# Optimization experiments

Hardware: AMD Instinct MI355X
Metric: run time of the kernel (lower is better)

Reference implementation:

```python
import jax, jax.numpy as jnp
import numpy as np

N_NODES = 50000
N_PAIRS = 625000
F = 128

def setup_inputs() -> dict:
    key = jax.random.key(0)
    k1, k2, k3, k4, k5 = jax.random.split(key, 5)
    x = jax.random.normal(k1, (N_NODES, F), dtype=jnp.float32)
    alpha_ij = jax.random.normal(k2, (N_PAIRS,), dtype=jnp.float32)
    idx_i = jax.random.randint(k3, (N_PAIRS,), 0, N_NODES, dtype=jnp.int32)
    idx_j = jax.random.randint(k4, (N_PAIRS,), 0, N_NODES, dtype=jnp.int32)
    # Dense(F, use_bias=False) kernel, shape (F_in, F_out)
    W = jax.random.normal(k5, (F, F), dtype=jnp.float32) / np.sqrt(F)
    return {"x": x, "alpha_ij": alpha_ij, "idx_i": idx_i, "idx_j": idx_j, "W": W}

def reference(x, alpha_ij, idx_i, idx_j, W):
    # dense projection on nodes (n,F) @ (F,F) -> (n,F)
    v = jnp.matmul(x, W)
    # gather neighbor values, scale by attention coeff: (n_pairs, F)
    msg = alpha_ij[:, None] * v[idx_j]
    # scatter-sum back to center atoms
    return jax.ops.segment_sum(msg, segment_ids=idx_i, num_segments=x.shape[0])
```

## Files before the change

kernel.cpp:

```cpp
#include <hip/hip_runtime.h>
#include <stdint.h>

#define FDIM 128
#define BR 64
#define SLOTS 48

typedef short  s8v   __attribute__((ext_vector_type(8)));
typedef float  f4v   __attribute__((ext_vector_type(4)));
typedef unsigned short u8v __attribute__((ext_vector_type(8)));

__device__ __forceinline__ unsigned short f2bf(float f) {
    union { float f; uint32_t u; } c; c.f = f;
    uint32_t u = c.u;
    return (unsigned short)((u + 0x7fffu + ((u >> 16) & 1u)) >> 16);
}
__device__ __forceinline__ float bflo2f(uint32_t g) {
    union { uint32_t u; float f; } c; c.u = g << 16; return c.f;
}
__device__ __forceinline__ float bfhi2f(uint32_t g) {
    union { uint32_t u; float f; } c; c.u = g & 0xffff0000u; return c.f;
}

__global__ __launch_bounds__(256) void prep(const float* __restrict__ W,
                                            unsigned short* __restrict__ Wt,
                                            int* __restrict__ cnt,
                                            int n_nodes) {
    int i = blockIdx.x * 256 + threadIdx.x;
    if (i < FDIM * FDIM) {
        int n = i & 127, k = i >> 7;
        Wt[n * FDIM + k] = f2bf(W[k * FDIM + n]);
    }
    if (i < n_nodes) cnt[i] = 0;
}

__global__ __launch_bounds__(256) void gemm_mfma(const float* __restrict__ x,
                                                 const unsigned short* __restrict__ Wt,
                                                 unsigned short* __restrict__ v,
                                                 int n_rows) {
    __shared__ unsigned short As[BR][FDIM + 8];
    __shared__ unsigned short Bs[FDIM][FDIM + 8];
    const int t = threadIdx.x;
    const int row0 = blockIdx.x * BR;

    {
        int n  = t >> 1;
        int cb = (t & 1) * 64;
        const unsigned short* src = Wt + (size_t)n * FDIM + cb;
#pragma unroll
        for (int it = 0; it < 8; ++it) {
            u8v wv = *(const u8v*)(src + it * 8);
            *(u8v*)(&Bs[n][cb + it * 8]) = wv;
        }
    }
    {
        int r  = t >> 2;
        int c0 = (t & 3) * 32;
        int grow = row0 + r;
        const float* src = x + (size_t)grow * FDIM + c0;
#pragma unroll
        for (int it = 0; it < 4; ++it) {
            float4 xa = make_float4(0.f, 0.f, 0.f, 0.f);
            float4 xb = make_float4(0.f, 0.f, 0.f, 0.f);
            if (grow < n_rows) {
                xa = *(const float4*)(src + it * 8);
                xb = *(const float4*)(src + it * 8 + 4);
            }
            u8v pk;
            pk[0] = f2bf(xa.x); pk[1] = f2bf(xa.y); pk[2] = f2bf(xa.z); pk[3] = f2bf(xa.w);
            pk[4] = f2bf(xb.x); pk[5] = f2bf(xb.y); pk[6] = f2bf(xb.z); pk[7] = f2bf(xb.w);
            *(u8v*)(&As[r][c0 + it * 8]) = pk;
        }
    }
    __syncthreads();

    const int w    = t >> 6;
    const int lane = t & 63;
    const int rt   = (w & 1) * 32;
    const int ct   = (w >> 1) * 64;
    const int lrow = lane & 15;
    const int kq   = (lane >> 4) * 8;

    f4v acc[2][4];
#pragma unroll
    for (int i = 0; i < 2; ++i)
#pragma unroll
        for (int j = 0; j < 4; ++j)
            acc[i][j] = (f4v){0.f, 0.f, 0.f, 0.f};

#pragma unroll
    for (int ks = 0; ks < 4; ++ks) {
        const int k0 = ks * 32 + kq;
        s8v a0 = *(const s8v*)(&As[rt + lrow][k0]);
        s8v a1 = *(const s8v*)(&As[rt + 16 + lrow][k0]);
        s8v b0 = *(const s8v*)(&Bs[ct + lrow][k0]);
        s8v b1 = *(const s8v*)(&Bs[ct + 16 + lrow][k0]);
        s8v b2 = *(const s8v*)(&Bs[ct + 32 + lrow][k0]);
        s8v b3 = *(const s8v*)(&Bs[ct + 48 + lrow][k0]);
        acc[0][0] = __builtin_amdgcn_mfma_f32_16x16x32_bf16(a0, b0, acc[0][0], 0, 0, 0);
        acc[0][1] = __builtin_amdgcn_mfma_f32_16x16x32_bf16(a0, b1, acc[0][1], 0, 0, 0);
        acc[0][2] = __builtin_amdgcn_mfma_f32_16x16x32_bf16(a0, b2, acc[0][2], 0, 0, 0);
        acc[0][3] = __builtin_amdgcn_mfma_f32_16x16x32_bf16(a0, b3, acc[0][3], 0, 0, 0);
        acc[1][0] = __builtin_amdgcn_mfma_f32_16x16x32_bf16(a1, b0, acc[1][0], 0, 0, 0);
        acc[1][1] = __builtin_amdgcn_mfma_f32_16x16x32_bf16(a1, b1, acc[1][1], 0, 0, 0);
        acc[1][2] = __builtin_amdgcn_mfma_f32_16x16x32_bf16(a1, b2, acc[1][2], 0, 0, 0);
        acc[1][3] = __builtin_amdgcn_mfma_f32_16x16x32_bf16(a1, b3, acc[1][3], 0, 0, 0);
    }

    const int quad = lane >> 4;
#pragma unroll
    for (int i = 0; i < 2; ++i) {
#pragma unroll
        for (int r = 0; r < 4; ++r) {
            int row = row0 + rt + i * 16 + quad * 4 + r;
            if (row < n_rows) {
#pragma unroll
                for (int j = 0; j < 4; ++j) {
                    int col = ct + j * 16 + lrow;
                    v[(size_t)row * FDIM + col] = f2bf(acc[i][j][r]);
                }
            }
        }
    }
}

__global__ __launch_bounds__(256) void scatter_direct(const int* __restrict__ idx_i,
                                                      const int* __restrict__ idx_j,
                                                      const float* __restrict__ alpha,
                                                      int* __restrict__ cnt,
                                                      int2* __restrict__ pairs,
                                                      int n_pairs) {
    int p = blockIdx.x * 256 + threadIdx.x;
    if (p >= n_pairs) return;
    int i   = idx_i[p];
    int pos = atomicAdd(&cnt[i], 1);
    if (pos < SLOTS) {
        int2 pr;
        pr.x = idx_j[p];
        pr.y = __float_as_int(alpha[p]);
        pairs[(size_t)i * SLOTS + pos] = pr;
    }
}

__global__ __launch_bounds__(256) void aggregate(const unsigned short* __restrict__ v,
                                                 const int* __restrict__ cnt,
                                                 const int2* __restrict__ pairs,
                                                 float* __restrict__ out,
                                                 int n_nodes) {
    const int node = blockIdx.x * 4 + (threadIdx.x >> 6);
    const int lane = threadIdx.x & 63;
    if (node >= n_nodes) return;

    int deg = cnt[node];
    deg = (deg > SLOTS) ? SLOTS : deg;
    const int2* pp = pairs + (size_t)node * SLOTS;

    float ax = 0.f, ay = 0.f;
    int k = 0;
    for (; k + 4 <= deg; k += 4) {
        int4 q0 = *(const int4*)(pp + k);
        int4 q1 = *(const int4*)(pp + k + 2);
        float a0 = __int_as_float(q0.y);
        float a1 = __int_as_float(q0.w);
        float a2 = __int_as_float(q1.y);
        float a3 = __int_as_float(q1.w);
        uint32_t g0 = *(const uint32_t*)(v + (size_t)q0.x * FDIM + lane * 2);
        uint32_t g1 = *(const uint32_t*)(v + (size_t)q0.z * FDIM + lane * 2);
        uint32_t g2 = *(const uint32_t*)(v + (size_t)q1.x * FDIM + lane * 2);
        uint32_t g3 = *(const uint32_t*)(v + (size_t)q1.z * FDIM + lane * 2);
        ax += a0 * bflo2f(g0) + a1 * bflo2f(g1);
        ay += a0 * bfhi2f(g0) + a1 * bfhi2f(g1);
        ax += a2 * bflo2f(g2) + a3 * bflo2f(g3);
        ay += a2 * bfhi2f(g2) + a3 * bfhi2f(g3);
    }
    if (k + 2 <= deg) {
        int4 q0 = *(const int4*)(pp + k);
        float a0 = __int_as_float(q0.y);
        float a1 = __int_as_float(q0.w);
        uint32_t g0 = *(const uint32_t*)(v + (size_t)q0.x * FDIM + lane * 2);
        uint32_t g1 = *(const uint32_t*)(v + (size_t)q0.z * FDIM + lane * 2);
        ax += a0 * bflo2f(g0) + a1 * bflo2f(g1);
        ay += a0 * bfhi2f(g0) + a1 * bfhi2f(g1);
        k += 2;
    }
    if (k < deg) {
        int2 p0 = pp[k];
        float a0 = __int_as_float(p0.y);
        uint32_t g0 = *(const uint32_t*)(v + (size_t)p0.x * FDIM + lane * 2);
        ax += a0 * bflo2f(g0);
        ay += a0 * bfhi2f(g0);
    }
    float2 r;
    r.x = ax;
    r.y = ay;
    *(float2*)(out + (size_t)node * FDIM + lane * 2) = r;
}

extern "C" void kernel_launch(void* const* d_in, const int* in_sizes, int n_in,
                              void* d_out, int out_size, void* d_ws, size_t ws_size,
                              hipStream_t stream) {
    const float* x     = (const float*)d_in[0];
    const float* alpha = (const float*)d_in[1];
    const int*   idx_i = (const int*)d_in[2];
    const int*   idx_j = (const int*)d_in[3];
    const float* W     = (const float*)d_in[4];

    const int n_nodes = in_sizes[0] / FDIM;
    const int n_pairs = in_sizes[1];

    char* ws = (char*)d_ws;
    size_t off = 0;
    auto carve = [&](size_t bytes) {
        char* p = ws + off;
        off += (bytes + 255) & ~(size_t)255;
        return p;
    };
    unsigned short* v  = (unsigned short*)carve((size_t)n_nodes * FDIM * sizeof(unsigned short));
    unsigned short* Wt = (unsigned short*)carve((size_t)FDIM * FDIM * sizeof(unsigned short));
    int*  cnt   = (int*) carve((size_t)n_nodes * sizeof(int));
    int2* pairs = (int2*)carve((size_t)n_nodes * SLOTS * sizeof(int2));
    float* out  = (float*)d_out;

    int pb = (max(n_nodes, FDIM * FDIM) + 255) / 256;
    prep<<<pb, 256, 0, stream>>>(W, Wt, cnt, n_nodes);

    int gblocks = (n_nodes + BR - 1) / BR;
    gemm_mfma<<<gblocks, 256, 0, stream>>>(x, Wt, v, n_nodes);

    int sblocks = (n_pairs + 255) / 256;
    scatter_direct<<<sblocks, 256, 0, stream>>>(idx_i, idx_j, alpha, cnt, pairs, n_pairs);

    int ablocks = (n_nodes + 3) / 4;
    aggregate<<<ablocks, 256, 0, stream>>>(v, cnt, pairs, out, n_nodes);
}
```

Baseline: 160.0 us.

## Fuse GEMM and scatter into one launch, read W directly from global

Merges the GEMM and the pair-scatter kernels into one launch, with blocks split by index: the first GB blocks do the projection and the rest bucket pairs into per-node slots. This lets the two independent phases overlap on the GPU and saves a launch. It also drops the shared-memory staging of the 32 KB bf16 weight tile and has each wave load its B fragments straight from global memory, relying on L1/L2 caching. That cuts LDS use and raises occupancy, at the cost of more global load traffic per MFMA step.

```diff
diff --git a/kernel.cpp b/kernel.cpp
--- a/kernel.cpp
+++ b/kernel.cpp
@@ -33,25 +33,35 @@
     if (i < n_nodes) cnt[i] = 0;
 }
 
-__global__ __launch_bounds__(256) void gemm_mfma(const float* __restrict__ x,
-                                                 const unsigned short* __restrict__ Wt,
-                                                 unsigned short* __restrict__ v,
-                                                 int n_rows) {
+__global__ __launch_bounds__(256) void fused_gemm_scatter(
+        const float* __restrict__ x,
+        const unsigned short* __restrict__ Wt,
+        unsigned short* __restrict__ v,
+        const int* __restrict__ idx_i,
+        const int* __restrict__ idx_j,
+        const float* __restrict__ alpha,
+        int* __restrict__ cnt,
+        int2* __restrict__ pairs,
+        int n_rows, int n_pairs, int GB) {
     __shared__ unsigned short As[BR][FDIM + 8];
-    __shared__ unsigned short Bs[FDIM][FDIM + 8];
+
+    if ((int)blockIdx.x >= GB) {
+        int p = (blockIdx.x - GB) * 256 + threadIdx.x;
+        if (p >= n_pairs) return;
+        int i   = idx_i[p];
+        int pos = atomicAdd(&cnt[i], 1);
+        if (pos < SLOTS) {
+            int2 pr;
+            pr.x = idx_j[p];
+            pr.y = __float_as_int(alpha[p]);
+            pairs[(size_t)i * SLOTS + pos] = pr;
+        }
+        return;
+    }
+
     const int t = threadIdx.x;
     const int row0 = blockIdx.x * BR;
 
-    {
-        int n  = t >> 1;
-        int cb = (t & 1) * 64;
-        const unsigned short* src = Wt + (size_t)n * FDIM + cb;
-#pragma unroll
-        for (int it = 0; it < 8; ++it) {
-            u8v wv = *(const u8v*)(src + it * 8);
-            *(u8v*)(&Bs[n][cb + it * 8]) = wv;
-        }
-    }
     {
         int r  = t >> 2;
         int c0 = (t & 3) * 32;
@@ -90,12 +100,13 @@
 #pragma unroll
     for (int ks = 0; ks < 4; ++ks) {
         const int k0 = ks * 32 + kq;
+        const unsigned short* wb = Wt + (size_t)(ct + lrow) * FDIM + k0;
+        s8v b0 = *(const s8v*)(wb);
+        s8v b1 = *(const s8v*)(wb + 16 * FDIM);
+        s8v b2 = *(const s8v*)(wb + 32 * FDIM);
+        s8v b3 = *(const s8v*)(wb + 48 * FDIM);
         s8v a0 = *(const s8v*)(&As[rt + lrow][k0]);
         s8v a1 = *(const s8v*)(&As[rt + 16 + lrow][k0]);
-        s8v b0 = *(const s8v*)(&Bs[ct + lrow][k0]);
-        s8v b1 = *(const s8v*)(&Bs[ct + 16 + lrow][k0]);
-        s8v b2 = *(const s8v*)(&Bs[ct + 32 + lrow][k0]);
-        s8v b3 = *(const s8v*)(&Bs[ct + 48 + lrow][k0]);
         acc[0][0] = __builtin_amdgcn_mfma_f32_16x16x32_bf16(a0, b0, acc[0][0], 0, 0, 0);
         acc[0][1] = __builtin_amdgcn_mfma_f32_16x16x32_bf16(a0, b1, acc[0][1], 0, 0, 0);
         acc[0][2] = __builtin_amdgcn_mfma_f32_16x16x32_bf16(a0, b2, acc[0][2], 0, 0, 0);
@@ -120,24 +131,6 @@
                 }
             }
         }
-    }
-}
-
-__global__ __launch_bounds__(256) void scatter_direct(const int* __restrict__ idx_i,
-                                                      const int* __restrict__ idx_j,
-                                                      const float* __restrict__ alpha,
-                                                      int* __restrict__ cnt,
-                                                      int2* __restrict__ pairs,
-                                                      int n_pairs) {
-    int p = blockIdx.x * 256 + threadIdx.x;
-    if (p >= n_pairs) return;
-    int i   = idx_i[p];
-    int pos = atomicAdd(&cnt[i], 1);
-    if (pos < SLOTS) {
-        int2 pr;
-        pr.x = idx_j[p];
-        pr.y = __float_as_int(alpha[p]);
-        pairs[(size_t)i * SLOTS + pos] = pr;
     }
 }
 
@@ -223,11 +216,10 @@
     int pb = (max(n_nodes, FDIM * FDIM) + 255) / 256;
     prep<<<pb, 256, 0, stream>>>(W, Wt, cnt, n_nodes);
 
-    int gblocks = (n_nodes + BR - 1) / BR;
-    gemm_mfma<<<gblocks, 256, 0, stream>>>(x, Wt, v, n_nodes);
-
-    int sblocks = (n_pairs + 255) / 256;
-    scatter_direct<<<sblocks, 256, 0, stream>>>(idx_i, idx_j, alpha, cnt, pairs, n_pairs);
+    int GB = (n_nodes + BR - 1) / BR;
+    int SB = (n_pairs + 255) / 256;
+    fused_gemm_scatter<<<GB + SB, 256, 0, stream>>>(x, Wt, v, idx_i, idx_j, alpha,
+                                                    cnt, pairs, n_nodes, n_pairs, GB);
 
     int ablocks = (n_nodes + 3) / 4;
     aggregate<<<ablocks, 256, 0, stream>>>(v, cnt, pairs, out, n_nodes);
```

Result: no change. 157.6 us (-1.5%).
